# Kernel optimization log

Measured on AMD Instinct MI355X. Metric: run time of the kernel, lower is better.

## Reference

```python
import jax, jax.numpy as jnp
import numpy as np

DIM = 256
N_NODES = 2000
BATCH = 64


def _build_tree(n, seed=0):
    # Contiguous-children encoding: struct[i] = (ch_start, ch_end) or (-1,-1) for leaves.
    # Children indices are always > parent index (BFS frontier allocation).
    rng = np.random.default_rng(seed)
    struct = np.full((n, 2), -1, dtype=np.int32)
    ptr = 1
    i = 0
    while ptr < n:
        k = int(rng.integers(0, 5))
        if i + 1 >= ptr:  # keep the frontier non-empty
            k = max(k, 1)
        k = min(k, n - ptr)
        if k > 0:
            struct[i] = (ptr, ptr + k)
            ptr += k
        i += 1
    return struct


def _level_schedule(struct):
    # depth 0 = leaves; parent depth = 1 + max(child depths). Children idx > parent idx.
    n = struct.shape[0]
    depth = np.zeros(n, dtype=np.int64)
    for i in range(n - 1, -1, -1):
        s, e = struct[i]
        if s != -1:
            depth[i] = 1 + depth[s:e].max()
    return [np.nonzero(depth == d)[0] for d in range(int(depth.max()) + 1)]


def setup_inputs() -> dict:
    key = jax.random.key(0)
    ks = jax.random.split(key, 3)
    struct = _build_tree(N_NODES)
    structure = jnp.asarray(np.broadcast_to(struct, (BATCH, N_NODES, 2)).copy())
    features = jax.random.normal(ks[0], (BATCH, N_NODES, DIM), dtype=jnp.float32)
    s_in = (2.0 / (DIM + DIM)) ** 0.5        # glorot-ish scale
    s_inner = (2.0 / (3 * DIM + DIM)) ** 0.5
    W_in = jax.random.normal(ks[1], (DIM, DIM), dtype=jnp.float32) * s_in
    b_in = jnp.zeros((DIM,), jnp.float32)
    W_inner = jax.random.normal(ks[2], (3 * DIM, DIM), dtype=jnp.float32) * s_inner
    b_inner = jnp.zeros((DIM,), jnp.float32)
    return {"structure": structure, "features": features, "W_in": W_in,
            "b_in": b_in, "W_inner": W_inner, "b_inner": b_inner}


def reference(structure, features, W_in, b_in, W_inner, b_inner):
    # Tree structure (int) is a compile-time constant: derive a level schedule host-side,
    # then run one batched segment-reduction + Dense per tree level (deepest first).
    struct = np.asarray(structure[0])  # shared across batch
    levels = _level_schedule(struct)
    B, N, dim = features.shape
    state = jnp.zeros((B, N, dim), features.dtype)

    # Leaves: sigmoid Dense on own features (all features are finite/valid here).
    leaves = levels[0]
    state = state.at[:, leaves].set(jax.nn.sigmoid(features[:, leaves] @ W_in + b_in))

    for nodes in levels[1:]:
        starts, ends = struct[nodes, 0], struct[nodes, 1]
        counts = ends - starts
        child_ids = np.concatenate([np.arange(s, e) for s, e in zip(starts, ends)])
        seg = np.repeat(np.arange(len(nodes)), counts)
        L = len(nodes)
        cs = state[:, child_ids].transpose(1, 0, 2)          # [C, B, dim]
        ssum = jax.ops.segment_sum(cs, seg, num_segments=L)  # [L, B, dim]
        smin = jax.ops.segment_min(cs, seg, num_segments=L)
        feat = features[:, nodes].transpose(1, 0, 2)         # node's own feature joins pooling
        cnt = jnp.asarray(counts + 1, features.dtype)[:, None, None]
        c_mean = (ssum + feat) / cnt
        c_min = jnp.minimum(smin, feat)
        # NOTE: the source computes c_max with reduce_mean (bug) -> kept for fidelity.
        h = jnp.concatenate([c_mean, c_mean, c_min], axis=-1)  # [L, B, 3*dim]
        new = jax.nn.sigmoid(h @ W_inner + b_inner)
        state = state.at[:, nodes].set(new.transpose(1, 0, 2))

    return state[:, 0]  # just_root_output=True -> [B, dim]
```

## Files before the change

kernel.cpp:

```cpp
#include <hip/hip_runtime.h>

#define NNODES 2000
#define BATCH  64
#define DIM    256
#define BLOCK  128
#define MAXGRID 1024

typedef __attribute__((ext_vector_type(8))) short  v8s;
typedef __attribute__((ext_vector_type(8))) __bf16 v8bf;
typedef __attribute__((ext_vector_type(4))) float  v4f;
typedef __attribute__((ext_vector_type(4))) int    v4i;

__device__ __forceinline__ short f2bf(float f) {
  unsigned u = __builtin_bit_cast(unsigned, f);
  u += 0x7FFFu + ((u >> 16) & 1u);
  return (short)(u >> 16);
}
__device__ __forceinline__ float bf2f(short s) {
  unsigned u = ((unsigned)(unsigned short)s) << 16;
  return __builtin_bit_cast(float, u);
}
__device__ __forceinline__ v4f mfma16(v8s a, v8s b, v4f c) {
  return __builtin_amdgcn_mfma_f32_16x16x32_bf16(
      __builtin_bit_cast(v8bf, a), __builtin_bit_cast(v8bf, b), c, 0, 0, 0);
}
__device__ __forceinline__ float sigmoidf(float x) {
  return __builtin_amdgcn_rcpf(1.0f + __builtin_amdgcn_exp2f(-1.4426950408889634f * x));
}

__global__ void prep_kernel(const float* __restrict__ W_in, const float* __restrict__ W_inner,
                            short* __restrict__ Wt_in, short* __restrict__ Wt_inner,
                            int* __restrict__ done) {
  int idx = blockIdx.x * blockDim.x + threadIdx.x;
  int stride = gridDim.x * blockDim.x;
  for (int i = idx; i < 256 * 256; i += stride) {
    int j = i >> 8, k = i & 255;
    Wt_in[j * 256 + k] = f2bf(W_in[k * 256 + j]);
  }
  for (int i = idx; i < 256 * 512; i += stride) {
    int j = i >> 9, k = i & 511;
    float v = W_inner[(k + 256) * 256 + j];
    if (k < 256) v += W_inner[k * 256 + j];
    Wt_inner[j * 512 + k] = f2bf(v);
  }
  for (int i = idx; i < 4 * NNODES; i += stride)
    __hip_atomic_store(&done[i], 0, __ATOMIC_RELAXED, __HIP_MEMORY_SCOPE_AGENT);
}

__launch_bounds__(BLOCK, 2)
__global__ void tree_kernel(const int* __restrict__ structure, const float* __restrict__ features,
                            const float* __restrict__ b_in, const float* __restrict__ b_inner,
                            const short* __restrict__ Wt_in, const short* __restrict__ Wt_inner,
                            short* __restrict__ state, int* done, float* __restrict__ out) {
  __shared__ short Xs[16 * 512];

  const int tid  = threadIdx.x;
  const int wave = tid >> 6;
  const int lane = tid & 63;
  const int ln15 = lane & 15;
  const int quad = lane >> 4;
  const int rl3  = ln15 & 7;

  const int bl  = tid >> 3;
  const int d0  = (tid & 7) << 5;
  const int swb = bl & 7;

  float bia_in[8], bia_nn[8];
  #pragma unroll
  for (int nt = 0; nt < 8; ++nt) {
    const int j = wave * 128 + nt * 16 + ln15;
    bia_in[nt] = b_in[j];
    bia_nn[nt] = b_inner[j];
  }

  for (int item = 4 * NNODES - 1 - (int)blockIdx.x; item >= 0; item -= (int)gridDim.x) {
    const int node = item >> 2;
    const int q    = item & 3;
    const int s = structure[2 * node];
    const int e = structure[2 * node + 1];
    const bool leaf = (s < 0);
    const int nc = e - s;
    const int K = leaf ? 256 : 512;
    const short* __restrict__ W = leaf ? Wt_in : Wt_inner;

    const int b = q * 16 + bl;
    const float* __restrict__ fp = features + ((size_t)b * NNODES + node) * DIM + d0;
    float4 pre[8];
    #pragma unroll
    for (int qq = 0; qq < 8; ++qq) pre[qq] = ((const float4*)fp)[qq];

    if (!leaf && wave == 0 && lane < nc) {
      int g = 0;
      while (__hip_atomic_load(&done[4 * (s + lane) + q],
                               __ATOMIC_RELAXED, __HIP_MEMORY_SCOPE_AGENT) == 0 &&
             g < (1 << 22)) {
        __builtin_amdgcn_s_sleep(1); ++g;
      }
    }
    __syncthreads();

    if (leaf) {
      #pragma unroll
      for (int dq = 0; dq < 4; ++dq) {
        const float4 f0 = pre[2 * dq];
        const float4 f1 = pre[2 * dq + 1];
        v8s o;
        o[0] = f2bf(f0.x); o[1] = f2bf(f0.y); o[2] = f2bf(f0.z); o[3] = f2bf(f0.w);
        o[4] = f2bf(f1.x); o[5] = f2bf(f1.y); o[6] = f2bf(f1.z); o[7] = f2bf(f1.w);
        const int ch = (d0 + dq * 8) >> 3;
        *(v8s*)&Xs[(bl << 9) + ((ch ^ swb) << 3)] = o;
      }
    } else {
      v4i cb[4][4];
      #pragma unroll
      for (int ci = 0; ci < 4; ++ci) {
        if (ci < nc) {
          const short* cp = state + ((size_t)(s + ci) * BATCH + b) * DIM + d0;
          #pragma unroll
          for (int dq = 0; dq < 4; ++dq)
            asm volatile("global_load_dwordx4 %0, %1, off sc0 sc1"
                         : "=v"(cb[ci][dq]) : "v"(cp + dq * 8));
        }
      }
      asm volatile("s_waitcnt vmcnt(0)" ::: "memory");
      __builtin_amdgcn_sched_barrier(0);

      const float inv = 1.0f / (float)(nc + 1);
      #pragma unroll
      for (int dq = 0; dq < 4; ++dq) {
        const float4 f0 = pre[2 * dq];
        const float4 f1 = pre[2 * dq + 1];
        float sm[8] = {f0.x, f0.y, f0.z, f0.w, f1.x, f1.y, f1.z, f1.w};
        float mn[8];
        #pragma unroll
        for (int qq = 0; qq < 8; ++qq) mn[qq] = sm[qq];
        #pragma unroll
        for (int ci = 0; ci < 4; ++ci) {
          if (ci < nc) {
            const v8s cv = __builtin_bit_cast(v8s, cb[ci][dq]);
            #pragma unroll
            for (int qq = 0; qq < 8; ++qq) {
              const float v = bf2f(cv[qq]);
              sm[qq] += v; mn[qq] = fminf(mn[qq], v);
            }
          }
        }
        v8s om, on;
        #pragma unroll
        for (int qq = 0; qq < 8; ++qq) { om[qq] = f2bf(sm[qq] * inv); on[qq] = f2bf(mn[qq]); }
        const int ch = (d0 + dq * 8) >> 3;
        *(v8s*)&Xs[(bl << 9) + ((ch ^ swb) << 3)]        = om;
        *(v8s*)&Xs[(bl << 9) + (((ch + 32) ^ swb) << 3)] = on;
      }
    }
    __syncthreads();

    v4f acc[8];
    #pragma unroll
    for (int nt = 0; nt < 8; ++nt) acc[nt] = v4f{0.f, 0.f, 0.f, 0.f};

    const short* __restrict__ Wp = W + (size_t)(wave * 128 + ln15) * K + quad * 8;
    const int nkc = K >> 5;
    v8s bcur[8];
    #pragma unroll
    for (int nt = 0; nt < 8; ++nt) bcur[nt] = *(const v8s*)(Wp + (size_t)nt * 16 * K);
    for (int kc = 0; kc < nkc; ++kc) {
      const int kn = (kc + 1 < nkc) ? kc + 1 : kc;
      v8s bnxt[8];
      #pragma unroll
      for (int nt = 0; nt < 8; ++nt) bnxt[nt] = *(const v8s*)(Wp + (size_t)nt * 16 * K + kn * 32);
      const v8s af = *(const v8s*)&Xs[(ln15 << 9) + (((kc * 4 + quad) ^ rl3) << 3)];
      #pragma unroll
      for (int nt = 0; nt < 8; ++nt)
        acc[nt] = mfma16(af, bcur[nt], acc[nt]);
      #pragma unroll
      for (int nt = 0; nt < 8; ++nt) bcur[nt] = bnxt[nt];
    }

    #pragma unroll
    for (int nt = 0; nt < 8; ++nt) {
      const int j = wave * 128 + nt * 16 + ln15;
      const float bs = leaf ? bia_in[nt] : bia_nn[nt];
      #pragma unroll
      for (int r = 0; r < 4; ++r) {
        const int bb = q * 16 + quad * 4 + r;
        const float v = sigmoidf(acc[nt][r] + bs);
        short* sp = state + ((size_t)node * BATCH + bb) * DIM + j;
        const int hv = (int)(unsigned short)f2bf(v);
        asm volatile("global_store_short %0, %1, off sc0 sc1" :: "v"(sp), "v"(hv));
        if (node == 0) out[bb * DIM + j] = v;
      }
    }

    asm volatile("s_waitcnt vmcnt(0)" ::: "memory");
    __syncthreads();
    if (tid == 0)
      __hip_atomic_store(&done[item], 1,
                         __ATOMIC_RELAXED, __HIP_MEMORY_SCOPE_AGENT);
  }
}

extern "C" void kernel_launch(void* const* d_in, const int* in_sizes, int n_in,
                              void* d_out, int out_size, void* d_ws, size_t ws_size,
                              hipStream_t stream) {
  const int*   structure = (const int*)d_in[0];
  const float* features  = (const float*)d_in[1];
  const float* W_in      = (const float*)d_in[2];
  const float* b_in      = (const float*)d_in[3];
  const float* W_inner   = (const float*)d_in[4];
  const float* b_inner   = (const float*)d_in[5];
  float* out = (float*)d_out;

  char* ws = (char*)d_ws;
  short* state = (short*)ws;
  size_t off = (size_t)NNODES * BATCH * DIM * 2;
  short* Wt_in = (short*)(ws + off);    off += 256 * 256 * 2;
  short* Wt_inner = (short*)(ws + off); off += 512 * 256 * 2;
  int* done = (int*)(ws + off);

  prep_kernel<<<dim3(256), dim3(256), 0, stream>>>(W_in, W_inner, Wt_in, Wt_inner, done);

  static int coop_grid = 0;
  if (coop_grid == 0) {
    int nb = 0;
    hipError_t err = hipOccupancyMaxActiveBlocksPerMultiprocessor(
        &nb, reinterpret_cast<const void*>(tree_kernel), BLOCK, 0);
    if (err != hipSuccess || nb < 1) nb = 1;
    long g = (long)nb * 256;
    if (g > MAXGRID) g = MAXGRID;
    coop_grid = (int)g;
  }

  void* args[9];
  args[0] = (void*)&structure;
  args[1] = (void*)&features;
  args[2] = (void*)&b_in;
  args[3] = (void*)&b_inner;
  args[4] = (void*)&Wt_in;
  args[5] = (void*)&Wt_inner;
  args[6] = (void*)&state;
  args[7] = (void*)&done;
  args[8] = (void*)&out;
  hipLaunchCooperativeKernel((void*)tree_kernel, dim3(coop_grid), dim3(BLOCK), args, 0, stream);
}
```

Before: 494.0 us.

## Stage outputs through LDS for vectorized state stores and remap load thread layout

```diff
diff --git a/kernel.cpp b/kernel.cpp
--- a/kernel.cpp
+++ b/kernel.cpp
@@ -5,6 +5,7 @@
 #define DIM    256
 #define BLOCK  128
 #define MAXGRID 1024
+#define TBLD   264
 
 typedef __attribute__((ext_vector_type(8))) short  v8s;
 typedef __attribute__((ext_vector_type(8))) __bf16 v8bf;
@@ -61,9 +62,8 @@
   const int quad = lane >> 4;
   const int rl3  = ln15 & 7;
 
-  const int bl  = tid >> 3;
-  const int d0  = (tid & 7) << 5;
-  const int swb = bl & 7;
+  const int rowb = tid >> 5;
+  const int ch   = tid & 31;
 
   float bia_in[8], bia_nn[8];
   #pragma unroll
@@ -83,11 +83,14 @@
     const int K = leaf ? 256 : 512;
     const short* __restrict__ W = leaf ? Wt_in : Wt_inner;
 
-    const int b = q * 16 + bl;
-    const float* __restrict__ fp = features + ((size_t)b * NNODES + node) * DIM + d0;
-    float4 pre[8];
-    #pragma unroll
-    for (int qq = 0; qq < 8; ++qq) pre[qq] = ((const float4*)fp)[qq];
+    float4 pf[4][2];
+    #pragma unroll
+    for (int g = 0; g < 4; ++g) {
+      const int b = q * 16 + rowb + 4 * g;
+      const float* __restrict__ fp = features + ((size_t)b * NNODES + node) * DIM + ch * 8;
+      pf[g][0] = ((const float4*)fp)[0];
+      pf[g][1] = ((const float4*)fp)[1];
+    }
 
     if (!leaf && wave == 0 && lane < nc) {
       int g = 0;
@@ -101,25 +104,26 @@
 
     if (leaf) {
       #pragma unroll
-      for (int dq = 0; dq < 4; ++dq) {
-        const float4 f0 = pre[2 * dq];
-        const float4 f1 = pre[2 * dq + 1];
+      for (int g = 0; g < 4; ++g) {
+        const int row = rowb + 4 * g;
+        const int sw  = row & 7;
+        const float4 f0 = pf[g][0], f1 = pf[g][1];
         v8s o;
         o[0] = f2bf(f0.x); o[1] = f2bf(f0.y); o[2] = f2bf(f0.z); o[3] = f2bf(f0.w);
         o[4] = f2bf(f1.x); o[5] = f2bf(f1.y); o[6] = f2bf(f1.z); o[7] = f2bf(f1.w);
-        const int ch = (d0 + dq * 8) >> 3;
-        *(v8s*)&Xs[(bl << 9) + ((ch ^ swb) << 3)] = o;
+        *(v8s*)&Xs[(row << 9) + ((ch ^ sw) << 3)] = o;
       }
     } else {
       v4i cb[4][4];
       #pragma unroll
       for (int ci = 0; ci < 4; ++ci) {
         if (ci < nc) {
-          const short* cp = state + ((size_t)(s + ci) * BATCH + b) * DIM + d0;
           #pragma unroll
-          for (int dq = 0; dq < 4; ++dq)
+          for (int g = 0; g < 4; ++g) {
+            const short* cp = state + ((size_t)(s + ci) * BATCH + q * 16 + rowb + 4 * g) * DIM + ch * 8;
             asm volatile("global_load_dwordx4 %0, %1, off sc0 sc1"
-                         : "=v"(cb[ci][dq]) : "v"(cp + dq * 8));
+                         : "=v"(cb[ci][g]) : "v"(cp));
+          }
         }
       }
       asm volatile("s_waitcnt vmcnt(0)" ::: "memory");
@@ -127,9 +131,10 @@
 
       const float inv = 1.0f / (float)(nc + 1);
       #pragma unroll
-      for (int dq = 0; dq < 4; ++dq) {
-        const float4 f0 = pre[2 * dq];
-        const float4 f1 = pre[2 * dq + 1];
+      for (int g = 0; g < 4; ++g) {
+        const int row = rowb + 4 * g;
+        const int sw  = row & 7;
+        const float4 f0 = pf[g][0], f1 = pf[g][1];
         float sm[8] = {f0.x, f0.y, f0.z, f0.w, f1.x, f1.y, f1.z, f1.w};
         float mn[8];
         #pragma unroll
@@ -137,7 +142,7 @@
         #pragma unroll
         for (int ci = 0; ci < 4; ++ci) {
           if (ci < nc) {
-            const v8s cv = __builtin_bit_cast(v8s, cb[ci][dq]);
+            const v8s cv = __builtin_bit_cast(v8s, cb[ci][g]);
             #pragma unroll
             for (int qq = 0; qq < 8; ++qq) {
               const float v = bf2f(cv[qq]);
@@ -148,9 +153,8 @@
         v8s om, on;
         #pragma unroll
         for (int qq = 0; qq < 8; ++qq) { om[qq] = f2bf(sm[qq] * inv); on[qq] = f2bf(mn[qq]); }
-        const int ch = (d0 + dq * 8) >> 3;
-        *(v8s*)&Xs[(bl << 9) + ((ch ^ swb) << 3)]        = om;
-        *(v8s*)&Xs[(bl << 9) + (((ch + 32) ^ swb) << 3)] = on;
+        *(v8s*)&Xs[(row << 9) + ((ch ^ sw) << 3)]          = om;
+        *(v8s*)&Xs[(row << 9) + (((ch + 32) ^ sw) << 3)]   = on;
       }
     }
     __syncthreads();
@@ -176,6 +180,7 @@
       #pragma unroll
       for (int nt = 0; nt < 8; ++nt) bcur[nt] = bnxt[nt];
     }
+    __syncthreads();
 
     #pragma unroll
     for (int nt = 0; nt < 8; ++nt) {
@@ -183,13 +188,20 @@
       const float bs = leaf ? bia_in[nt] : bia_nn[nt];
       #pragma unroll
       for (int r = 0; r < 4; ++r) {
-        const int bb = q * 16 + quad * 4 + r;
+        const int bb = quad * 4 + r;
         const float v = sigmoidf(acc[nt][r] + bs);
-        short* sp = state + ((size_t)node * BATCH + bb) * DIM + j;
-        const int hv = (int)(unsigned short)f2bf(v);
-        asm volatile("global_store_short %0, %1, off sc0 sc1" :: "v"(sp), "v"(hv));
-        if (node == 0) out[bb * DIM + j] = v;
-      }
+        Xs[bb * TBLD + j] = f2bf(v);
+        if (node == 0) out[(q * 16 + bb) * DIM + j] = v;
+      }
+    }
+    __syncthreads();
+
+    #pragma unroll
+    for (int g = 0; g < 4; ++g) {
+      const int row = rowb + 4 * g;
+      const v4i val = *(const v4i*)&Xs[row * TBLD + ch * 8];
+      short* sp = state + ((size_t)node * BATCH + q * 16 + row) * DIM + ch * 8;
+      asm volatile("global_store_dwordx4 %0, %1, off sc0 sc1" :: "v"(sp), "v"(val));
     }
 
     asm volatile("s_waitcnt vmcnt(0)" ::: "memory");
```

New measurement: 472.6 us. 4.3% less time.
